# Kernel optimization log

Measured on AMD Instinct MI355X. Metric: run time of the kernel, lower is better.

The kernel has to match this reference:

```python
import jax, jax.numpy as jnp
import numpy as np

B, S, H, QS, VS = 32, 2048, 1024, 1024, 2048


def setup_inputs() -> dict:
    key = jax.random.key(0)
    k1, k2, k3, k4, k5, k6 = jax.random.split(key, 6)
    query = jax.random.normal(k1, (B, QS), dtype=jnp.float32)
    proj_key = jax.random.normal(k2, (B, S, H), dtype=jnp.float32)
    value = jax.random.normal(k3, (B, S, VS), dtype=jnp.float32)
    mask = jax.random.randint(k4, (B, 1, S), 0, 2, dtype=jnp.int32)
    Wq = jax.random.normal(k5, (QS, H), dtype=jnp.float32) * (1.0 / np.sqrt(QS))
    v_energy = jax.random.normal(k6, (H,), dtype=jnp.float32) * (1.0 / np.sqrt(H))
    return {"query": query, "proj_key": proj_key, "value": value,
            "mask": mask, "Wq": Wq, "v_energy": v_energy}


def reference(query, proj_key, value, mask, Wq, v_energy):
    # query_layer: [B, QS] @ [QS, H] -> [B, H], then unsqueeze to [B, 1, H]
    q = (query @ Wq)[:, None, :]
    # energy: v . tanh(q + proj_key) -> scores [B, S] -> [B, 1, S]
    scores = jnp.einsum('bsh,h->bs', jnp.tanh(q + proj_key), v_energy)[:, None, :]
    scores = jnp.where(mask == 0, -jnp.inf, scores)
    alphas = jax.nn.softmax(scores, axis=-1)            # [B, 1, S]
    context = jnp.einsum('bts,sv->btv', alphas[0:0], value[0:0]) if False else jnp.matmul(alphas, value)  # [B, 1, VS]
    return (context, alphas)
```

## Files before the change

### kernel.cpp

```cpp
#include <hip/hip_runtime.h>
#include <math.h>

#define Bb 32
#define Ss 2048
#define Hh 1024
#define QSq 1024
#define VSv 2048
#define SCH 32

typedef float fx4 __attribute__((ext_vector_type(4)));

__device__ __forceinline__ float fast_tanh(float x) {
    float xc = fminf(fmaxf(x, -10.f), 10.f);
    float e  = __expf(2.f * xc);
    return 1.f - 2.f * __builtin_amdgcn_rcpf(e + 1.f);
}

__device__ __forceinline__ fx4 ntload4(const float* p) {
    return __builtin_nontemporal_load((const fx4*)p);
}
__device__ __forceinline__ void ntstore4(float* p, fx4 v) {
    __builtin_nontemporal_store(v, (fx4*)p);
}

__global__ void k_qproj(const float* __restrict__ query,
                        const float* __restrict__ Wq,
                        float* __restrict__ q) {
    __shared__ float qrow[QSq];
    const int b   = blockIdx.x >> 2;
    const int h0  = (blockIdx.x & 3) * 256;
    const int tid = threadIdx.x;
    for (int i = tid; i < QSq; i += 256) qrow[i] = query[b * QSq + i];
    __syncthreads();
    const int h = h0 + tid;
    float a0 = 0.f, a1 = 0.f, a2 = 0.f, a3 = 0.f;
#pragma unroll 8
    for (int qs = 0; qs < QSq; qs += 4) {
        a0 += qrow[qs + 0] * Wq[(size_t)(qs + 0) * Hh + h];
        a1 += qrow[qs + 1] * Wq[(size_t)(qs + 1) * Hh + h];
        a2 += qrow[qs + 2] * Wq[(size_t)(qs + 2) * Hh + h];
        a3 += qrow[qs + 3] * Wq[(size_t)(qs + 3) * Hh + h];
    }
    q[b * Hh + h] = (a0 + a1) + (a2 + a3);
}

__device__ __forceinline__ float dot_tanh4(const float* sh_q, const float* sh_v,
                                           int h, fx4 p) {
    const float4 qv = *(const float4*)&sh_q[h];
    const float4 vv = *(const float4*)&sh_v[h];
    float a;
    a  = vv.x * fast_tanh(qv.x + p.x);
    a += vv.y * fast_tanh(qv.y + p.y);
    a += vv.z * fast_tanh(qv.z + p.z);
    a += vv.w * fast_tanh(qv.w + p.w);
    return a;
}

__global__ void k_scores(const float* __restrict__ pk,
                         const int*   __restrict__ mask,
                         const float* __restrict__ q,
                         const float* __restrict__ ve,
                         float* __restrict__ scores) {
    __shared__ float sh_q[Hh];
    __shared__ float sh_v[Hh];
    const int tid = threadIdx.x;
    const int b   = blockIdx.x / (Ss / 8);
    const int s0  = (blockIdx.x % (Ss / 8)) * 8;
    for (int i = tid; i < Hh; i += 256) { sh_q[i] = q[b * Hh + i]; sh_v[i] = ve[i]; }
    __syncthreads();
    const int wave = tid >> 6, lane = tid & 63;
    const int s = s0 + wave * 2;
    const int m0 = mask[b * Ss + s], m1 = mask[b * Ss + s + 1];
    if (lane == 0) {
        if (!m0) scores[b * Ss + s]     = -INFINITY;
        if (!m1) scores[b * Ss + s + 1] = -INFINITY;
    }
    if (!m0 && !m1) return;
    const float* r0 = pk + (size_t)(b * Ss + s) * Hh;
    const float* r1 = r0 + Hh;
    float acc0 = 0.f, acc1 = 0.f;
    if (m0 && m1) {
        fx4 P0[4], P1[4];
#pragma unroll
        for (int j = 0; j < 4; ++j) P0[j] = ntload4(r0 + (j * 64 + lane) * 4);
#pragma unroll
        for (int j = 0; j < 4; ++j) P1[j] = ntload4(r1 + (j * 64 + lane) * 4);
#pragma unroll
        for (int j = 0; j < 4; ++j) {
            const int h = (j * 64 + lane) * 4;
            acc0 += dot_tanh4(sh_q, sh_v, h, P0[j]);
            acc1 += dot_tanh4(sh_q, sh_v, h, P1[j]);
        }
    } else {
        const float* r = m0 ? r0 : r1;
        fx4 P[4];
#pragma unroll
        for (int j = 0; j < 4; ++j) P[j] = ntload4(r + (j * 64 + lane) * 4);
        float acc = 0.f;
#pragma unroll
        for (int j = 0; j < 4; ++j) {
            const int h = (j * 64 + lane) * 4;
            acc += dot_tanh4(sh_q, sh_v, h, P[j]);
        }
        if (m0) acc0 = acc; else acc1 = acc;
    }
#pragma unroll
    for (int off = 32; off; off >>= 1) {
        acc0 += __shfl_xor(acc0, off);
        acc1 += __shfl_xor(acc1, off);
    }
    if (lane == 0) {
        if (m0) scores[b * Ss + s]     = acc0;
        if (m1) scores[b * Ss + s + 1] = acc1;
    }
}

__global__ void k_softmax(const float* __restrict__ scores,
                          float* __restrict__ alphas,
                          int*   __restrict__ lidx,
                          float* __restrict__ lal,
                          int*   __restrict__ lcount) {
    const int b = blockIdx.x, tid = threadIdx.x;
    const int wave = tid >> 6, lane = tid & 63;
    __shared__ float sred[4];
    __shared__ float ssum[4];
    __shared__ int   swt[4];
    float v[8];
    *(float4*)&v[0] = *(const float4*)&scores[b * Ss + tid * 8];
    *(float4*)&v[4] = *(const float4*)&scores[b * Ss + tid * 8 + 4];
    float m = -INFINITY;
#pragma unroll
    for (int i = 0; i < 8; ++i) m = fmaxf(m, v[i]);
#pragma unroll
    for (int off = 32; off; off >>= 1) m = fmaxf(m, __shfl_xor(m, off));
    if (lane == 0) sred[wave] = m;
    __syncthreads();
    m = fmaxf(fmaxf(sred[0], sred[1]), fmaxf(sred[2], sred[3]));
    float e[8];
    float sum = 0.f;
#pragma unroll
    for (int i = 0; i < 8; ++i) { e[i] = __expf(v[i] - m); sum += e[i]; }
#pragma unroll
    for (int off = 32; off; off >>= 1) sum += __shfl_xor(sum, off);
    if (lane == 0) ssum[wave] = sum;
    __syncthreads();
    sum = (ssum[0] + ssum[1]) + (ssum[2] + ssum[3]);
    const float inv = 1.f / sum;
    float a[8];
#pragma unroll
    for (int i = 0; i < 8; ++i) a[i] = e[i] * inv;
    ntstore4(&alphas[b * Ss + tid * 8],     *(fx4*)&a[0]);
    ntstore4(&alphas[b * Ss + tid * 8 + 4], *(fx4*)&a[4]);

    int c = 0;
#pragma unroll
    for (int i = 0; i < 8; ++i) c += (v[i] > -INFINITY) ? 1 : 0;
    int incl = c;
#pragma unroll
    for (int off = 1; off < 64; off <<= 1) {
        int y = __shfl_up(incl, off);
        if (lane >= off) incl += y;
    }
    if (lane == 63) swt[wave] = incl;
    __syncthreads();
    int base = 0;
#pragma unroll
    for (int w = 0; w < 4; ++w) base += (w < wave) ? swt[w] : 0;
    int pos = base + incl - c;
#pragma unroll
    for (int i = 0; i < 8; ++i) {
        if (v[i] > -INFINITY) {
            lidx[b * Ss + pos] = tid * 8 + i;
            lal[b * Ss + pos]  = a[i];
            ++pos;
        }
    }
    if (tid == 0) lcount[b] = swt[0] + swt[1] + swt[2] + swt[3];
}

__global__ void k_ctx_partial(const float* __restrict__ value,
                              const int*   __restrict__ lidx,
                              const float* __restrict__ lal,
                              const int*   __restrict__ lcount,
                              float* __restrict__ part) {
    __shared__ int   sidx[64];
    __shared__ float sal[64];
    const int tid = threadIdx.x;
    const int b   = blockIdx.x / SCH;
    const int sc  = blockIdx.x % SCH;
    const int c0  = tid * 4;
    const int count = lcount[b];
    const int chunk = (count + SCH - 1) / SCH;
    const int beg = sc * chunk;
    const int end = min(beg + chunk, count);
    const int n   = end - beg;
    if (tid < n) {
        sidx[tid] = lidx[b * Ss + beg + tid];
        sal[tid]  = lal[b * Ss + beg + tid];
    }
    __syncthreads();
    const float* vb = value + (size_t)b * Ss * VSv;
    fx4 accA = {0.f, 0.f, 0.f, 0.f};
    fx4 accB = {0.f, 0.f, 0.f, 0.f};
    int i = 0;
    for (; i + 8 <= n; i += 8) {
        fx4   wa[8], wb[8];
        float a[8];
#pragma unroll
        for (int k = 0; k < 8; ++k) {
            const float* rp = vb + (size_t)sidx[i + k] * VSv + c0;
            wa[k] = ntload4(rp);
            wb[k] = ntload4(rp + 1024);
            a[k]  = sal[i + k];
        }
#pragma unroll
        for (int k = 0; k < 8; ++k) {
            accA += a[k] * wa[k];
            accB += a[k] * wb[k];
        }
    }
    for (; i < n; ++i) {
        const float a = sal[i];
        const float* rp = vb + (size_t)sidx[i] * VSv + c0;
        accA += a * ntload4(rp);
        accB += a * ntload4(rp + 1024);
    }
    float* pr = part + ((size_t)(b * SCH + sc)) * VSv + c0;
    *(fx4*)pr          = accA;
    *(fx4*)(pr + 1024) = accB;
}

__global__ void k_ctx_reduce(const float* __restrict__ part,
                             float* __restrict__ out) {
    const int idx = blockIdx.x * 256 + threadIdx.x;
    const int b = idx / (VSv / 4), v4 = idx % (VSv / 4);
    fx4 acc = {0.f, 0.f, 0.f, 0.f};
#pragma unroll
    for (int c = 0; c < SCH; ++c) {
        acc += ntload4(part + ((size_t)(b * SCH + c)) * VSv + v4 * 4);
    }
    *(fx4*)(out + (size_t)b * VSv + v4 * 4) = acc;
}

extern "C" void kernel_launch(void* const* d_in, const int* in_sizes, int n_in,
                              void* d_out, int out_size, void* d_ws, size_t ws_size,
                              hipStream_t stream) {
    const float* query    = (const float*)d_in[0];
    const float* proj_key = (const float*)d_in[1];
    const float* value    = (const float*)d_in[2];
    const int*   mask     = (const int*)d_in[3];
    const float* Wq       = (const float*)d_in[4];
    const float* v_energy = (const float*)d_in[5];

    float* out        = (float*)d_out;
    float* ctx_out    = out;
    float* alphas_out = out + Bb * VSv;

    float* ws     = (float*)d_ws;
    float* q      = ws;
    float* scores = q + Bb * Hh;
    float* lal    = scores + Bb * Ss;
    int*   lidx   = (int*)(lal + Bb * Ss);
    int*   lcount = lidx + Bb * Ss;
    float* part   = (float*)(lcount + 32);

    hipLaunchKernelGGL(k_qproj,       dim3(Bb * 4),              dim3(256), 0, stream, query, Wq, q);
    hipLaunchKernelGGL(k_scores,      dim3(Bb * (Ss / 8)),       dim3(256), 0, stream, proj_key, mask, q, v_energy, scores);
    hipLaunchKernelGGL(k_softmax,     dim3(Bb),                  dim3(256), 0, stream, scores, alphas_out, lidx, lal, lcount);
    hipLaunchKernelGGL(k_ctx_partial, dim3(Bb * SCH),            dim3(256), 0, stream, value, lidx, lal, lcount, part);
    hipLaunchKernelGGL(k_ctx_reduce,  dim3((Bb * VSv / 4) / 256), dim3(256), 0, stream, part, ctx_out);
}
```

Before: 102.4 us.

## Compact live mask rows per block in scores kernel and retune grids

Each scores block now covers 64 sequence positions. It builds a compact list of unmasked rows with a wave ballot, and each wave processes pairs of live rows. This avoids waves sitting idle on masked rows and cuts the number of blocks that reload q and v_energy into shared memory. The change also doubles the context split count and reshapes the qproj and ctx_reduce launches to smaller blocks. These add more partial-sum traffic in exchange for more parallelism, and the larger scores blocks lose some grid-level parallelism.

```diff
diff --git a/kernel.cpp b/kernel.cpp
--- a/kernel.cpp
+++ b/kernel.cpp
@@ -6,7 +6,8 @@
 #define Hh 1024
 #define QSq 1024
 #define VSv 2048
-#define SCH 32
+#define SCH 64
+#define SB  64
 
 typedef float fx4 __attribute__((ext_vector_type(4)));
 
@@ -27,10 +28,11 @@
                         const float* __restrict__ Wq,
                         float* __restrict__ q) {
     __shared__ float qrow[QSq];
-    const int b   = blockIdx.x >> 2;
-    const int h0  = (blockIdx.x & 3) * 256;
+    const int b   = blockIdx.x >> 3;
+    const int h0  = (blockIdx.x & 7) * 128;
     const int tid = threadIdx.x;
-    for (int i = tid; i < QSq; i += 256) qrow[i] = query[b * QSq + i];
+    for (int i = tid; i < QSq / 4; i += 128)
+        ((float4*)qrow)[i] = ((const float4*)(query + b * QSq))[i];
     __syncthreads();
     const int h = h0 + tid;
     float a0 = 0.f, a1 = 0.f, a2 = 0.f, a3 = 0.f;
@@ -63,55 +65,50 @@
                          float* __restrict__ scores) {
     __shared__ float sh_q[Hh];
     __shared__ float sh_v[Hh];
+    __shared__ unsigned char slist[SB];
+    __shared__ int snlive;
     const int tid = threadIdx.x;
-    const int b   = blockIdx.x / (Ss / 8);
-    const int s0  = (blockIdx.x % (Ss / 8)) * 8;
-    for (int i = tid; i < Hh; i += 256) { sh_q[i] = q[b * Hh + i]; sh_v[i] = ve[i]; }
-    __syncthreads();
     const int wave = tid >> 6, lane = tid & 63;
-    const int s = s0 + wave * 2;
-    const int m0 = mask[b * Ss + s], m1 = mask[b * Ss + s + 1];
-    if (lane == 0) {
-        if (!m0) scores[b * Ss + s]     = -INFINITY;
-        if (!m1) scores[b * Ss + s + 1] = -INFINITY;
-    }
-    if (!m0 && !m1) return;
-    const float* r0 = pk + (size_t)(b * Ss + s) * Hh;
-    const float* r1 = r0 + Hh;
-    float acc0 = 0.f, acc1 = 0.f;
-    if (m0 && m1) {
+    const int b   = blockIdx.x / (Ss / SB);
+    const int s0  = (blockIdx.x % (Ss / SB)) * SB;
+    ((float4*)sh_q)[tid] = ((const float4*)(q + b * Hh))[tid];
+    ((float4*)sh_v)[tid] = ((const float4*)ve)[tid];
+    if (wave == 0) {
+        const int m = mask[b * Ss + s0 + lane];
+        const unsigned long long bal = __ballot(m != 0);
+        if (!m) scores[b * Ss + s0 + lane] = -INFINITY;
+        else slist[__popcll(bal & ((1ull << lane) - 1ull))] = (unsigned char)lane;
+        if (lane == 0) snlive = __popcll(bal);
+    }
+    __syncthreads();
+    const int nlive = snlive;
+    for (int p = wave * 2; p < nlive; p += 8) {
+        const int sA = s0 + slist[p];
+        const bool dual = (p + 1 < nlive);
+        const int sB = dual ? s0 + slist[p + 1] : sA;
+        const float* r0 = pk + (size_t)(b * Ss + sA) * Hh;
+        const float* r1 = pk + (size_t)(b * Ss + sB) * Hh;
         fx4 P0[4], P1[4];
 #pragma unroll
         for (int j = 0; j < 4; ++j) P0[j] = ntload4(r0 + (j * 64 + lane) * 4);
 #pragma unroll
         for (int j = 0; j < 4; ++j) P1[j] = ntload4(r1 + (j * 64 + lane) * 4);
+        float acc0 = 0.f, acc1 = 0.f;
 #pragma unroll
         for (int j = 0; j < 4; ++j) {
             const int h = (j * 64 + lane) * 4;
             acc0 += dot_tanh4(sh_q, sh_v, h, P0[j]);
             acc1 += dot_tanh4(sh_q, sh_v, h, P1[j]);
         }
-    } else {
-        const float* r = m0 ? r0 : r1;
-        fx4 P[4];
-#pragma unroll
-        for (int j = 0; j < 4; ++j) P[j] = ntload4(r + (j * 64 + lane) * 4);
-        float acc = 0.f;
-#pragma unroll
-        for (int j = 0; j < 4; ++j) {
-            const int h = (j * 64 + lane) * 4;
-            acc += dot_tanh4(sh_q, sh_v, h, P[j]);
-        }
-        if (m0) acc0 = acc; else acc1 = acc;
-    }
-#pragma unroll
-    for (int off = 32; off; off >>= 1) {
-        acc0 += __shfl_xor(acc0, off);
-        acc1 += __shfl_xor(acc1, off);
-    }
-    if (lane == 0) {
-        if (m0) scores[b * Ss + s]     = acc0;
-        if (m1) scores[b * Ss + s + 1] = acc1;
+#pragma unroll
+        for (int off = 32; off; off >>= 1) {
+            acc0 += __shfl_xor(acc0, off);
+            acc1 += __shfl_xor(acc1, off);
+        }
+        if (lane == 0) {
+            scores[b * Ss + sA] = acc0;
+            if (dual) scores[b * Ss + sB] = acc1;
+        }
     }
 }
 
@@ -232,10 +229,10 @@
 
 __global__ void k_ctx_reduce(const float* __restrict__ part,
                              float* __restrict__ out) {
-    const int idx = blockIdx.x * 256 + threadIdx.x;
+    const int idx = blockIdx.x * 64 + threadIdx.x;
     const int b = idx / (VSv / 4), v4 = idx % (VSv / 4);
     fx4 acc = {0.f, 0.f, 0.f, 0.f};
-#pragma unroll
+#pragma unroll 8
     for (int c = 0; c < SCH; ++c) {
         acc += ntload4(part + ((size_t)(b * SCH + c)) * VSv + v4 * 4);
     }
@@ -264,9 +261,9 @@
     int*   lcount = lidx + Bb * Ss;
     float* part   = (float*)(lcount + 32);
 
-    hipLaunchKernelGGL(k_qproj,       dim3(Bb * 4),              dim3(256), 0, stream, query, Wq, q);
-    hipLaunchKernelGGL(k_scores,      dim3(Bb * (Ss / 8)),       dim3(256), 0, stream, proj_key, mask, q, v_energy, scores);
-    hipLaunchKernelGGL(k_softmax,     dim3(Bb),                  dim3(256), 0, stream, scores, alphas_out, lidx, lal, lcount);
-    hipLaunchKernelGGL(k_ctx_partial, dim3(Bb * SCH),            dim3(256), 0, stream, value, lidx, lal, lcount, part);
-    hipLaunchKernelGGL(k_ctx_reduce,  dim3((Bb * VSv / 4) / 256), dim3(256), 0, stream, part, ctx_out);
-}
+    hipLaunchKernelGGL(k_qproj,       dim3(Bb * 8),             dim3(128), 0, stream, query, Wq, q);
+    hipLaunchKernelGGL(k_scores,      dim3(Bb * (Ss / SB)),     dim3(256), 0, stream, proj_key, mask, q, v_energy, scores);
+    hipLaunchKernelGGL(k_softmax,     dim3(Bb),                 dim3(256), 0, stream, scores, alphas_out, lidx, lal, lcount);
+    hipLaunchKernelGGL(k_ctx_partial, dim3(Bb * SCH),           dim3(256), 0, stream, value, lidx, lal, lcount, part);
+    hipLaunchKernelGGL(k_ctx_reduce,  dim3(Bb * VSv / 4 / 64),  dim3(64),  0, stream, part, ctx_out);
+}
```

Result: slower. 108.0 us (+5.5%).

## Fuse context reduction into partial kernel via last-block atomic counter

Applied to the files above, without the earlier changes.

Removes the separate k_ctx_reduce launch. Each batch's last-finishing partial block, found with an atomic counter that the softmax kernel resets, sums the SCH partial rows and writes the context output. Also regrids the q projection to more, smaller blocks and vectorises the shared-memory loads of q and v_energy. This saves one kernel launch and its tail, at the cost of threadfences, an atomic per block, and a serial reduction done by only 32 blocks.

```diff
diff --git a/kernel.cpp b/kernel.cpp
--- a/kernel.cpp
+++ b/kernel.cpp
@@ -27,10 +27,11 @@
                         const float* __restrict__ Wq,
                         float* __restrict__ q) {
     __shared__ float qrow[QSq];
-    const int b   = blockIdx.x >> 2;
-    const int h0  = (blockIdx.x & 3) * 256;
+    const int b   = blockIdx.x >> 3;
+    const int h0  = (blockIdx.x & 7) * 128;
     const int tid = threadIdx.x;
-    for (int i = tid; i < QSq; i += 256) qrow[i] = query[b * QSq + i];
+    for (int i = tid; i < QSq / 4; i += 128)
+        ((float4*)qrow)[i] = ((const float4*)(query + b * QSq))[i];
     __syncthreads();
     const int h = h0 + tid;
     float a0 = 0.f, a1 = 0.f, a2 = 0.f, a3 = 0.f;
@@ -66,7 +67,8 @@
     const int tid = threadIdx.x;
     const int b   = blockIdx.x / (Ss / 8);
     const int s0  = (blockIdx.x % (Ss / 8)) * 8;
-    for (int i = tid; i < Hh; i += 256) { sh_q[i] = q[b * Hh + i]; sh_v[i] = ve[i]; }
+    ((float4*)sh_q)[tid] = ((const float4*)(q + b * Hh))[tid];
+    ((float4*)sh_v)[tid] = ((const float4*)ve)[tid];
     __syncthreads();
     const int wave = tid >> 6, lane = tid & 63;
     const int s = s0 + wave * 2;
@@ -119,9 +121,11 @@
                           float* __restrict__ alphas,
                           int*   __restrict__ lidx,
                           float* __restrict__ lal,
-                          int*   __restrict__ lcount) {
+                          int*   __restrict__ lcount,
+                          int*   __restrict__ bcount) {
     const int b = blockIdx.x, tid = threadIdx.x;
     const int wave = tid >> 6, lane = tid & 63;
+    if (tid == 0) bcount[b] = 0;
     __shared__ float sred[4];
     __shared__ float ssum[4];
     __shared__ int   swt[4];
@@ -182,9 +186,12 @@
                               const int*   __restrict__ lidx,
                               const float* __restrict__ lal,
                               const int*   __restrict__ lcount,
-                              float* __restrict__ part) {
+                              float* __restrict__ part,
+                              int*   __restrict__ bcount,
+                              float* __restrict__ ctx_out) {
     __shared__ int   sidx[64];
     __shared__ float sal[64];
+    __shared__ int   sdone;
     const int tid = threadIdx.x;
     const int b   = blockIdx.x / SCH;
     const int sc  = blockIdx.x % SCH;
@@ -193,7 +200,7 @@
     const int chunk = (count + SCH - 1) / SCH;
     const int beg = sc * chunk;
     const int end = min(beg + chunk, count);
-    const int n   = end - beg;
+    const int n   = max(end - beg, 0);
     if (tid < n) {
         sidx[tid] = lidx[b * Ss + beg + tid];
         sal[tid]  = lal[b * Ss + beg + tid];
@@ -228,18 +235,23 @@
     float* pr = part + ((size_t)(b * SCH + sc)) * VSv + c0;
     *(fx4*)pr          = accA;
     *(fx4*)(pr + 1024) = accB;
-}
-
-__global__ void k_ctx_reduce(const float* __restrict__ part,
-                             float* __restrict__ out) {
-    const int idx = blockIdx.x * 256 + threadIdx.x;
-    const int b = idx / (VSv / 4), v4 = idx % (VSv / 4);
-    fx4 acc = {0.f, 0.f, 0.f, 0.f};
-#pragma unroll
+
+    __threadfence();
+    if (tid == 0) sdone = atomicAdd(&bcount[b], 1);
+    __syncthreads();
+    if (sdone != SCH - 1) return;
+    __threadfence();
+    fx4 fA = {0.f, 0.f, 0.f, 0.f};
+    fx4 fB = {0.f, 0.f, 0.f, 0.f};
+    const float* pb = part + (size_t)b * SCH * VSv + c0;
+#pragma unroll 8
     for (int c = 0; c < SCH; ++c) {
-        acc += ntload4(part + ((size_t)(b * SCH + c)) * VSv + v4 * 4);
-    }
-    *(fx4*)(out + (size_t)b * VSv + v4 * 4) = acc;
+        fA += ntload4(pb + (size_t)c * VSv);
+        fB += ntload4(pb + (size_t)c * VSv + 1024);
+    }
+    float* outp = ctx_out + (size_t)b * VSv + c0;
+    *(fx4*)outp          = fA;
+    *(fx4*)(outp + 1024) = fB;
 }
 
 extern "C" void kernel_launch(void* const* d_in, const int* in_sizes, int n_in,
@@ -262,11 +274,11 @@
     float* lal    = scores + Bb * Ss;
     int*   lidx   = (int*)(lal + Bb * Ss);
     int*   lcount = lidx + Bb * Ss;
-    float* part   = (float*)(lcount + 32);
-
-    hipLaunchKernelGGL(k_qproj,       dim3(Bb * 4),              dim3(256), 0, stream, query, Wq, q);
-    hipLaunchKernelGGL(k_scores,      dim3(Bb * (Ss / 8)),       dim3(256), 0, stream, proj_key, mask, q, v_energy, scores);
-    hipLaunchKernelGGL(k_softmax,     dim3(Bb),                  dim3(256), 0, stream, scores, alphas_out, lidx, lal, lcount);
-    hipLaunchKernelGGL(k_ctx_partial, dim3(Bb * SCH),            dim3(256), 0, stream, value, lidx, lal, lcount, part);
-    hipLaunchKernelGGL(k_ctx_reduce,  dim3((Bb * VSv / 4) / 256), dim3(256), 0, stream, part, ctx_out);
-}
+    int*   bcount = lcount + 32;
+    float* part   = (float*)(bcount + 32);
+
+    hipLaunchKernelGGL(k_qproj,       dim3(Bb * 8),         dim3(128), 0, stream, query, Wq, q);
+    hipLaunchKernelGGL(k_scores,      dim3(Bb * (Ss / 8)),  dim3(256), 0, stream, proj_key, mask, q, v_energy, scores);
+    hipLaunchKernelGGL(k_softmax,     dim3(Bb),             dim3(256), 0, stream, scores, alphas_out, lidx, lal, lcount, bcount);
+    hipLaunchKernelGGL(k_ctx_partial, dim3(Bb * SCH),       dim3(256), 0, stream, value, lidx, lal, lcount, part, bcount, ctx_out);
+}
```

After: 324.1 us. 216% more time.
